# Performance work log

Hardware: AMD Instinct MI355X
Metric: run time of the kernel (lower is better)

Reference implementation:

```python
import jax, jax.numpy as jnp
import numpy as np

B, T, N, D_IN = 2, 64, 64, 512
HID, L, H = 256, 2, 4
C = HID // H  # 64 per-head channels
NEG_SLOPE = 0.2
LN_EPS = 1e-5


def setup_inputs() -> dict:
    key = jax.random.key(0)
    ks = jax.random.split(key, 8)
    s_in = 1.0 / np.sqrt(D_IN)
    s_h = 1.0 / np.sqrt(HID)
    s_c = 1.0 / np.sqrt(C)
    return {
        "x": jax.random.normal(ks[0], (B, T, N, D_IN), jnp.float32),
        "person_mask": jax.random.randint(ks[1], (B, T, N), 0, 2) > 0,
        "W_in": (jax.random.normal(ks[2], (D_IN, HID)) * s_in).astype(jnp.float32),
        "b_in": jnp.zeros((HID,), jnp.float32),
        "Wl": (jax.random.normal(ks[3], (L, HID, HID)) * s_h).astype(jnp.float32),
        "bl": jnp.zeros((L, HID), jnp.float32),
        "Wr": (jax.random.normal(ks[4], (L, HID, HID)) * s_h).astype(jnp.float32),
        "br": jnp.zeros((L, HID), jnp.float32),
        "att": (jax.random.normal(ks[5], (L, H, C)) * s_c).astype(jnp.float32),
        "out_bias": jnp.zeros((L, HID), jnp.float32),
        "ln_scale": jnp.ones((L, HID), jnp.float32),
        "ln_bias": jnp.zeros((L, HID), jnp.float32),
    }


def _layernorm(x, g, b):
    mu = jnp.mean(x, axis=-1, keepdims=True)
    var = jnp.mean(jnp.square(x - mu), axis=-1, keepdims=True)
    return (x - mu) * jax.lax.rsqrt(var + LN_EPS) * g + b


def _gatv2_layer(h, allowed, Wl, bl, Wr, br, att, ob):
    # h: [bt, N, HID]; allowed: [bt, N, N] bool (edge j->i at [b,i,j])
    bt, n, _ = h.shape
    xl = (h @ Wl + bl).reshape(bt, n, H, C)  # source features (messages)
    xr = (h @ Wr + br).reshape(bt, n, H, C)  # target features
    # GATv2 logit: e_ij = a . leaky_relu(xr_i + xl_j), per head
    s = xr[:, :, None, :, :] + xl[:, None, :, :, :]  # [bt, i, j, H, C]
    e = jnp.einsum('bijhc,hc->bijh', jax.nn.leaky_relu(s, NEG_SLOPE), att)
    e = jnp.where(allowed[..., None], e, -1e9)
    alpha = jax.nn.softmax(e, axis=2)  # segment softmax over incoming edges j
    out = jnp.einsum('bijh,bjhc->bihc', alpha, xl)  # weighted scatter-sum
    return out.reshape(bt, n, H * C) + ob


def _forward(x, person_mask, W_in, b_in, Wl, bl, Wr, br, att, out_bias, ln_scale, ln_bias):
    b, t, n, _ = x.shape
    bt = b * t
    h = (x @ W_in + b_in).reshape(bt, n, HID)
    m = person_mask.reshape(bt, n)
    # edges: all pairs among masked nodes (incl. diag) + self loops for every node
    allowed = (m[:, :, None] & m[:, None, :]) | jnp.eye(n, dtype=bool)[None]
    hi = h
    for li in range(L):
        res = hi
        g = _gatv2_layer(hi, allowed, Wl[li], bl[li], Wr[li], br[li], att[li], out_bias[li])
        g = jax.nn.elu(g)  # dropout is identity in eval mode
        g = _layernorm(g, ln_scale[li], ln_bias[li])
        hi = g + res  # use_residual=True
        hi = jnp.where(m[:, :, None], hi, 0.0)
    # graphs with <=1 masked node are skipped (pass through projected features)
    keep = (jnp.sum(m, axis=-1) > 1)[:, None, None]
    out = jnp.where(keep, hi, h)
    return out.reshape(b, t, n, HID)


def reference(x, person_mask, W_in, b_in, Wl, bl, Wr, br, att, out_bias, ln_scale, ln_bias):
    return _forward(x, person_mask, W_in, b_in, Wl, bl, Wr, br, att, out_bias, ln_scale, ln_bias)
```

## Files before the change

kernel.cpp:

```cpp
#include <hip/hip_runtime.h>
#include <hip/hip_bf16.h>

#define BT_G   128
#define NND    64
#define D_IN_  512
#define HID_   256
#define NH     4
#define NCH    64
#define NROWS  8192
#define LN_EPS_    1e-5f

typedef __hip_bfloat16 bf16;
typedef __attribute__((ext_vector_type(8))) short short8;
typedef __attribute__((ext_vector_type(4))) float float4v;

__device__ __forceinline__ float toF(bf16 x) { return __bfloat162float(x); }

__global__ __launch_bounds__(256) void transpose_all_kernel(
    const float* __restrict__ W_in, const float* __restrict__ Wl,
    const float* __restrict__ Wr, const unsigned int* __restrict__ mw,
    bf16* __restrict__ WTin, bf16* __restrict__ WlrT, int* __restrict__ mout) {
    const int z = blockIdx.z;
    const int tid = threadIdx.x;
    if (z == 5) {
        if (blockIdx.x || blockIdx.y) return;
        __shared__ int okInt, okF32, okB16, okByte;
        if (tid == 0) { okInt = 1; okF32 = 1; okB16 = 1; okByte = 1; }
        __syncthreads();
        int aI = 1, aF = 1, aB = 1, aC = 1;
        for (int i = tid; i < 2048; i += 256) {
            unsigned w = mw[i];
            aI &= (w <= 1u);
            aF &= (w == 0u || w == 0x3F800000u);
            unsigned lo = w & 0xFFFFu, hi = w >> 16;
            aB &= ((lo == 0u || lo == 0x3F80u) && (hi == 0u || hi == 0x3F80u));
            aC &= (((w | (w >> 8) | (w >> 16) | (w >> 24)) & 0xFEu) == 0u);
        }
        if (!aI) atomicAnd(&okInt, 0);
        if (!aF) atomicAnd(&okF32, 0);
        if (!aB) atomicAnd(&okB16, 0);
        if (!aC) atomicAnd(&okByte, 0);
        __syncthreads();
        const int layout = (okInt || okF32) ? 0 : (okB16 ? 2 : (okByte ? 3 : 0));
        for (int i = tid; i < NROWS; i += 256) {
            int v;
            if (layout == 2)      v = (((const unsigned short*)mw)[i] != 0);
            else if (layout == 3) v = (((const unsigned char*)mw)[i] != 0);
            else                  v = (mw[i] != 0u);
            mout[i] = v;
        }
        return;
    }
    __shared__ float t[32][33];
    const float* src; bf16* dst; int K;
    if (z == 0)      { src = W_in;                 dst = WTin;                    K = 512; }
    else if (z <= 2) { src = Wl + (z - 1) * 65536; dst = WlrT + (z - 1) * 131072; K = 256; }
    else             { src = Wr + (z - 3) * 65536; dst = WlrT + (z - 3) * 131072 + 256 * 256; K = 256; }
    const int n0 = blockIdx.x * 32, k0 = blockIdx.y * 32;
    if (k0 >= K) return;
    const int tx = tid & 31, ty = tid >> 5;
    #pragma unroll
    for (int i = 0; i < 4; ++i)
        t[ty + 8 * i][tx] = src[(size_t)(k0 + ty + 8 * i) * 256 + n0 + tx];
    __syncthreads();
    #pragma unroll
    for (int i = 0; i < 4; ++i)
        dst[(size_t)(n0 + ty + 8 * i) * K + k0 + tx] =
            __float2bfloat16(t[tx][ty + 8 * i]);
}

__global__ __launch_bounds__(256) void gemm_in_kernel(
    const float* __restrict__ A, const bf16* __restrict__ BT,
    const float* __restrict__ bias, float* __restrict__ Cf,
    bf16* __restrict__ Cb16)
{
    __shared__ bf16 As[64 * 72];
    __shared__ bf16 Bs[64 * 72];
    const int tid  = threadIdx.x;
    const int wave = tid >> 6, lane = tid & 63;
    const int quad = lane >> 4, l16 = lane & 15;
    const int m0 = blockIdx.y * 64, n0 = blockIdx.x * 64;
    const int wm = (wave & 1) * 32, wn = (wave >> 1) * 32;
    float4v acc[2][2] = {};
    const int r  = tid >> 2;
    const int cq = (tid & 3) * 16;

    for (int k0 = 0; k0 < D_IN_; k0 += 64) {
        const float* sa = A + (size_t)(m0 + r) * D_IN_ + k0 + cq;
        const float4 f0 = *(const float4*)(sa);
        const float4 f1 = *(const float4*)(sa + 4);
        const float4 f2 = *(const float4*)(sa + 8);
        const float4 f3 = *(const float4*)(sa + 12);
        const bf16* sb = BT + (size_t)(n0 + r) * D_IN_ + k0 + cq;
        const float4 b0 = *(const float4*)(sb);
        const float4 b1 = *(const float4*)(sb + 8);
        union { bf16 h[16]; float4 v[2]; } u;
        u.h[0]=__float2bfloat16(f0.x); u.h[1]=__float2bfloat16(f0.y);
        u.h[2]=__float2bfloat16(f0.z); u.h[3]=__float2bfloat16(f0.w);
        u.h[4]=__float2bfloat16(f1.x); u.h[5]=__float2bfloat16(f1.y);
        u.h[6]=__float2bfloat16(f1.z); u.h[7]=__float2bfloat16(f1.w);
        u.h[8]=__float2bfloat16(f2.x); u.h[9]=__float2bfloat16(f2.y);
        u.h[10]=__float2bfloat16(f2.z); u.h[11]=__float2bfloat16(f2.w);
        u.h[12]=__float2bfloat16(f3.x); u.h[13]=__float2bfloat16(f3.y);
        u.h[14]=__float2bfloat16(f3.z); u.h[15]=__float2bfloat16(f3.w);
        __syncthreads();
        *(float4*)(&As[r * 72 + cq])     = u.v[0];
        *(float4*)(&As[r * 72 + cq + 8]) = u.v[1];
        *(float4*)(&Bs[r * 72 + cq])     = b0;
        *(float4*)(&Bs[r * 72 + cq + 8]) = b1;
        __syncthreads();
        #pragma unroll
        for (int kk = 0; kk < 64; kk += 32) {
            short8 af[2], bf2[2];
            #pragma unroll
            for (int mi = 0; mi < 2; ++mi)
                af[mi] = *(const short8*)(&As[(wm + mi * 16 + l16) * 72 + kk + quad * 8]);
            #pragma unroll
            for (int ni = 0; ni < 2; ++ni)
                bf2[ni] = *(const short8*)(&Bs[(wn + ni * 16 + l16) * 72 + kk + quad * 8]);
            #pragma unroll
            for (int mi = 0; mi < 2; ++mi)
                #pragma unroll
                for (int ni = 0; ni < 2; ++ni)
                    acc[mi][ni] = __builtin_amdgcn_mfma_f32_16x16x32_bf16(
                        af[mi], bf2[ni], acc[mi][ni], 0, 0, 0);
        }
    }
    #pragma unroll
    for (int ni = 0; ni < 2; ++ni) {
        const int col = n0 + wn + ni * 16 + l16;
        const float bv = bias[col];
        #pragma unroll
        for (int mi = 0; mi < 2; ++mi)
            #pragma unroll
            for (int rr = 0; rr < 4; ++rr) {
                const int row = m0 + wm + mi * 16 + quad * 4 + rr;
                const float v = acc[mi][ni][rr] + bv;
                Cf[(size_t)row * HID_ + col] = v;
                Cb16[(size_t)row * HID_ + col] = __float2bfloat16(v);
            }
    }
}

__global__ __launch_bounds__(256) void gemm_mfma_kernel(
    const bf16* __restrict__ A, const bf16* __restrict__ BT,
    const float* __restrict__ bias0, const float* __restrict__ bias1,
    float* __restrict__ Ca, float* __restrict__ Cbf, int M, int K)
{
    __shared__ bf16 As[128 * 72];
    __shared__ bf16 Bs[64 * 72];
    const int tid  = threadIdx.x;
    const int wave = tid >> 6, lane = tid & 63;
    const int quad = lane >> 4, l16 = lane & 15;
    const int m0 = blockIdx.y * 128, n0g = blockIdx.x * 64;
    const int wm = (wave & 1) * 64, wn = (wave >> 1) * 32;
    float4v acc[4][2] = {};
    const int r  = tid >> 2;
    const int cq = (tid & 3) * 16;

    for (int k0 = 0; k0 < K; k0 += 64) {
        const bf16* sa0 = A  + (size_t)(m0 + r) * K + k0 + cq;
        const bf16* sa1 = sa0 + (size_t)64 * K;
        const bf16* sb  = BT + (size_t)(n0g + r) * K + k0 + cq;
        const float4 a00 = *(const float4*)(sa0);
        const float4 a01 = *(const float4*)(sa0 + 8);
        const float4 a10 = *(const float4*)(sa1);
        const float4 a11 = *(const float4*)(sa1 + 8);
        const float4 b0  = *(const float4*)(sb);
        const float4 b1  = *(const float4*)(sb + 8);
        __syncthreads();
        *(float4*)(&As[r * 72 + cq])            = a00;
        *(float4*)(&As[r * 72 + cq + 8])        = a01;
        *(float4*)(&As[(r + 64) * 72 + cq])     = a10;
        *(float4*)(&As[(r + 64) * 72 + cq + 8]) = a11;
        *(float4*)(&Bs[r * 72 + cq])            = b0;
        *(float4*)(&Bs[r * 72 + cq + 8])        = b1;
        __syncthreads();
        #pragma unroll
        for (int kk = 0; kk < 64; kk += 32) {
            short8 af[4], bf2[2];
            #pragma unroll
            for (int mi = 0; mi < 4; ++mi)
                af[mi] = *(const short8*)(&As[(wm + mi * 16 + l16) * 72 + kk + quad * 8]);
            #pragma unroll
            for (int ni = 0; ni < 2; ++ni)
                bf2[ni] = *(const short8*)(&Bs[(wn + ni * 16 + l16) * 72 + kk + quad * 8]);
            #pragma unroll
            for (int mi = 0; mi < 4; ++mi)
                #pragma unroll
                for (int ni = 0; ni < 2; ++ni)
                    acc[mi][ni] = __builtin_amdgcn_mfma_f32_16x16x32_bf16(
                        af[mi], bf2[ni], acc[mi][ni], 0, 0, 0);
        }
    }
    const bool loHalf = (n0g < 256);
    float* Co = loHalf ? Ca : Cbf;
    const float* bp = loHalf ? bias0 : bias1;
    const int cbase = loHalf ? n0g : (n0g - 256);
    #pragma unroll
    for (int ni = 0; ni < 2; ++ni) {
        const int col = cbase + wn + ni * 16 + l16;
        const float bv = bp[col];
        #pragma unroll
        for (int mi = 0; mi < 4; ++mi)
            #pragma unroll
            for (int rr = 0; rr < 4; ++rr) {
                const int row = m0 + wm + mi * 16 + quad * 4 + rr;
                Co[(size_t)row * 256 + col] = acc[mi][ni][rr] + bv;
            }
    }
}

__global__ __launch_bounds__(256) void attn_kernel(
    const float* xl, const float* xr, const float* att,
    const int* msk, float* g)
{
    __shared__ float xls [64][68];
    __shared__ float xlsT[64][68];
    __shared__ float xrsT[64][68];
    __shared__ float esT [64][68];
    __shared__ float av[64], P[64], Q[64], mxf[64], inv[64];
    __shared__ float pmax[4][64], psum[4][64];
    __shared__ int   ms[64];
    const int tid  = threadIdx.x;
    const int head = blockIdx.x, gr = blockIdx.y;
    const int ti = tid >> 4, tj = tid & 15;
    const int i0 = ti * 4, j0 = tj * 4;
    const float* xlg = xl + (size_t)gr * NND * HID_ + head * NCH;
    const float* xrg = xr + (size_t)gr * NND * HID_ + head * NCH;

    {
        const int r  = tid >> 2;
        const int c0 = (tid & 3) * 16;
        float a[4][4], b[4][4];
        #pragma unroll
        for (int k = 0; k < 4; ++k) {
            *(float4*)a[k] = *(const float4*)(xlg + r * HID_ + c0 + 4 * k);
            *(float4*)b[k] = *(const float4*)(xrg + r * HID_ + c0 + 4 * k);
        }
        #pragma unroll
        for (int k = 0; k < 4; ++k)
            *(float4*)&xls[r][c0 + 4 * k] = *(float4*)a[k];
        #pragma unroll
        for (int k = 0; k < 4; ++k)
            #pragma unroll
            for (int w = 0; w < 4; ++w) {
                xlsT[c0 + 4 * k + w][r] = a[k][w];
                xrsT[c0 + 4 * k + w][r] = b[k][w];
            }
    }
    if (tid < 64) {
        av[tid] = att[head * NCH + tid];
        ms[tid] = msk[gr * NND + tid];
    }
    __syncthreads();

    float aa[4][4] = {};
    for (int c = 0; c < 64; ++c) {
        float xr4[4], xl4[4];
        *(float4*)xr4 = *(const float4*)&xrsT[c][i0];
        *(float4*)xl4 = *(const float4*)&xlsT[c][j0];
        const float a = av[c];
        #pragma unroll
        for (int y = 0; y < 4; ++y)
            #pragma unroll
            for (int x = 0; x < 4; ++x)
                aa[y][x] = fmaf(a, fabsf(xr4[y] + xl4[x]), aa[y][x]);
    }
    if (tid < 64) {
        float s = 0.f;
        for (int c = 0; c < 64; ++c) s = fmaf(av[c], xrsT[c][tid], s);
        P[tid] = s;
    } else if (tid < 128) {
        const int j = tid - 64;
        float s = 0.f;
        for (int c = 0; c < 64; ++c) s = fmaf(av[c], xlsT[c][j], s);
        Q[j] = s;
    }
    __syncthreads();

    {
        float Pv[4], Qv[4]; int mi4[4], mj4[4];
        #pragma unroll
        for (int y = 0; y < 4; ++y) { Pv[y] = P[i0 + y]; mi4[y] = ms[i0 + y]; }
        #pragma unroll
        for (int x = 0; x < 4; ++x) { Qv[x] = Q[j0 + x]; mj4[x] = ms[j0 + x]; }
        #pragma unroll
        for (int x = 0; x < 4; ++x) {
            float col[4];
            #pragma unroll
            for (int y = 0; y < 4; ++y) {
                float e = fmaf(0.4f, aa[y][x], 0.6f * (Pv[y] + Qv[x]));
                const bool allowed = (mi4[y] && mj4[x]) || (i0 + y == j0 + x);
                col[y] = allowed ? e : -1e9f;
            }
            *(float4*)&esT[j0 + x][i0] = *(float4*)col;
        }
    }
    __syncthreads();

    {
        const int si = tid & 63, q = tid >> 6;
        float mx = -1e30f;
        #pragma unroll
        for (int k = 0; k < 16; ++k) mx = fmaxf(mx, esT[16 * q + k][si]);
        pmax[q][si] = mx;
    }
    __syncthreads();
    if (tid < 64)
        mxf[tid] = fmaxf(fmaxf(pmax[0][tid], pmax[1][tid]),
                         fmaxf(pmax[2][tid], pmax[3][tid]));
    __syncthreads();
    {
        const int si = tid & 63, q = tid >> 6;
        const float mx = mxf[si];
        float s = 0.f;
        #pragma unroll
        for (int k = 0; k < 16; ++k) {
            const float ev = __expf(esT[16 * q + k][si] - mx);
            esT[16 * q + k][si] = ev;
            s += ev;
        }
        psum[q][si] = s;
    }
    __syncthreads();
    if (tid < 64)
        inv[tid] = 1.f / (psum[0][tid] + psum[1][tid] + psum[2][tid] + psum[3][tid]);
    __syncthreads();

    {
        const int c0 = j0;
        float oa[4][4] = {};
        for (int j = 0; j < 64; ++j) {
            float al[4], xv[4];
            *(float4*)al = *(const float4*)&esT[j][i0];
            *(float4*)xv = *(const float4*)&xls[j][c0];
            #pragma unroll
            for (int y = 0; y < 4; ++y)
                #pragma unroll
                for (int x = 0; x < 4; ++x)
                    oa[y][x] = fmaf(al[y], xv[x], oa[y][x]);
        }
        #pragma unroll
        for (int y = 0; y < 4; ++y) {
            const float iv = inv[i0 + y];
            float o[4];
            #pragma unroll
            for (int x = 0; x < 4; ++x) o[x] = oa[y][x] * iv;
            float* go = g + (size_t)(gr * NND + i0 + y) * HID_ + head * NCH + c0;
            *(float4*)go = *(float4*)o;
        }
    }
}

__global__ __launch_bounds__(256) void epilogue_kernel(
    const float* __restrict__ g, const float* res,
    const float* __restrict__ ob, const float* __restrict__ lns,
    const float* __restrict__ lnb, const int* __restrict__ msk,
    float* hout, bf16* hb, int finalSel)
{
    const int lane = threadIdx.x & 63;
    const int wave = threadIdx.x >> 6;
    const int m = blockIdx.x * 4 + wave;
    if (finalSel) {
        const int gr = m >> 6;
        const int mv = msk[gr * NND + lane];
        const unsigned long long bal = __ballot(mv != 0);
        if (__popcll(bal) <= 1) return;
    }
    const float* grow = g + (size_t)m * HID_;
    float v[4];
    float sum = 0.f;
    #pragma unroll
    for (int q = 0; q < 4; ++q) {
        const int c = q * 64 + lane;
        float x = grow[c] + ob[c];
        x = x > 0.f ? x : (__expf(x) - 1.f);
        v[q] = x; sum += x;
    }
    #pragma unroll
    for (int off = 1; off < 64; off <<= 1) sum += __shfl_xor(sum, off);
    const float mu = sum * (1.f / 256.f);
    float vs = 0.f;
    #pragma unroll
    for (int q = 0; q < 4; ++q) { const float d = v[q] - mu; vs += d * d; }
    #pragma unroll
    for (int off = 1; off < 64; off <<= 1) vs += __shfl_xor(vs, off);
    const float rstd = rsqrtf(vs * (1.f / 256.f) + LN_EPS_);
    const int mnode = msk[m];
    const float* rrow = res + (size_t)m * HID_;
    float* ho = hout + (size_t)m * HID_;
    #pragma unroll
    for (int q = 0; q < 4; ++q) {
        const int c = q * 64 + lane;
        float y = (v[q] - mu) * rstd * lns[c] + lnb[c];
        y += rrow[c];
        y = mnode ? y : 0.f;
        ho[c] = y;
        if (hb) hb[(size_t)m * HID_ + c] = __float2bfloat16(y);
    }
}

extern "C" void kernel_launch(void* const* d_in, const int* in_sizes, int n_in,
                              void* d_out, int out_size, void* d_ws, size_t ws_size,
                              hipStream_t stream) {
    const float* x    = (const float*)d_in[0];
    const float* W_in = (const float*)d_in[2];
    const float* b_in = (const float*)d_in[3];
    const float* Wl   = (const float*)d_in[4];
    const float* bl   = (const float*)d_in[5];
    const float* Wr   = (const float*)d_in[6];
    const float* br   = (const float*)d_in[7];
    const float* att  = (const float*)d_in[8];
    const float* ob   = (const float*)d_in[9];
    const float* lns  = (const float*)d_in[10];
    const float* lnb  = (const float*)d_in[11];
    float* out = (float*)d_out;

    char* w = (char*)d_ws;
    int*   mcan = (int*)w;                      w += 32768;
    float* h    = (float*)w;                    w += (size_t)NROWS * HID_ * 4;
    float* xlb  = (float*)w;                    w += (size_t)NROWS * HID_ * 4;
    float* xrb  = (float*)w;                    w += (size_t)NROWS * HID_ * 4;
    bf16*  hxb  = (bf16*)w;                     w += (size_t)NROWS * HID_ * 2;
    bf16*  WTin = (bf16*)w;                     w += (size_t)D_IN_ * HID_ * 2;
    bf16*  WlrT = (bf16*)w;
    float* gb   = xrb;

    transpose_all_kernel<<<dim3(8, 16, 6), 256, 0, stream>>>(
        W_in, Wl, Wr, (const unsigned int*)d_in[1], WTin, WlrT, mcan);

    gemm_in_kernel<<<dim3(HID_ / 64, NROWS / 64), 256, 0, stream>>>(
        x, WTin, b_in, out, hxb);

    for (int li = 0; li < 2; ++li) {
        const float* resf = (li == 0) ? out : h;
        gemm_mfma_kernel<<<dim3(512 / 64, NROWS / 128), 256, 0, stream>>>(
            hxb, WlrT + (size_t)li * 512 * HID_, bl + li * HID_, br + li * HID_,
            xlb, xrb, NROWS, HID_);
        attn_kernel<<<dim3(NH, BT_G), 256, 0, stream>>>(
            xlb, xrb, att + li * NH * NCH, mcan, gb);
        if (li == 0) {
            epilogue_kernel<<<NROWS / 4, 256, 0, stream>>>(
                gb, resf, ob, lns, lnb, mcan, h, hxb, 0);
        } else {
            epilogue_kernel<<<NROWS / 4, 256, 0, stream>>>(
                gb, resf, ob + HID_, lns + HID_, lnb + HID_, mcan,
                out, (bf16*)nullptr, 1);
        }
    }

    (void)in_sizes; (void)n_in; (void)out_size; (void)ws_size;
}
```

Measured before the change: 176.8 us.

## Fuse all stages into one persistent cooperative kernel with grid syncs

Replaces the eight separate launches (transpose, input GEMM, and per-layer GEMM, attention and epilogue) with a single cooperative kernel of 256 blocks. Each stage runs as a grid-stride loop over work units, separated by grid.sync, with a union of per-stage shared-memory layouts. The goal is to remove per-launch overhead and tail gaps between kernels. In exchange it adds grid-wide barrier cost, caps the grid at one persistent wave of blocks, and sizes shared memory for the largest stage. The mask loading is also simplified to assume a 32-bit element layout, and a multi-kernel fallback path is kept in case the cooperative launch fails.

Result: slower. 458.9 us (+159.5%).

```diff
diff --git a/kernel.cpp b/kernel.cpp
--- a/kernel.cpp
+++ b/kernel.cpp
@@ -1,123 +1,112 @@
 #include <hip/hip_runtime.h>
 #include <hip/hip_bf16.h>
-
-#define BT_G   128
+#include <hip/hip_cooperative_groups.h>
+
+namespace cg = cooperative_groups;
+
 #define NND    64
 #define D_IN_  512
 #define HID_   256
 #define NH     4
 #define NCH    64
 #define NROWS  8192
-#define LN_EPS_    1e-5f
+#define LN_EPS_ 1e-5f
+#define CGRID  256
 
 typedef __hip_bfloat16 bf16;
 typedef __attribute__((ext_vector_type(8))) short short8;
 typedef __attribute__((ext_vector_type(4))) float float4v;
 
-__device__ __forceinline__ float toF(bf16 x) { return __bfloat162float(x); }
-
-__global__ __launch_bounds__(256) void transpose_all_kernel(
-    const float* __restrict__ W_in, const float* __restrict__ Wl,
-    const float* __restrict__ Wr, const unsigned int* __restrict__ mw,
-    bf16* __restrict__ WTin, bf16* __restrict__ WlrT, int* __restrict__ mout) {
-    const int z = blockIdx.z;
+struct TrS { float t[32][33]; };
+struct G1S { bf16 As[64 * 72]; bf16 Bs[64 * 72]; };
+struct G2S { bf16 As[128 * 72]; bf16 Bs[64 * 72]; };
+struct AtS {
+    float xls [64][68];
+    float xlsT[64][68];
+    float xrsT[64][68];
+    float esT [64][68];
+    float av[64], P[64], Q[64], mxf[64], inv[64];
+    float pmax[4][64], psum[4][64];
+    int   ms[64];
+};
+union SharedU { TrS tr; G1S g1; G2S g2; AtS at; };
+
+
+__device__ __forceinline__ void phase_transpose(
+    int u, TrS& sh, const float* W_in, const float* Wl, const float* Wr,
+    const unsigned int* mw, bf16* WTin, bf16* WlrT, int* mcan)
+{
     const int tid = threadIdx.x;
-    if (z == 5) {
-        if (blockIdx.x || blockIdx.y) return;
-        __shared__ int okInt, okF32, okB16, okByte;
-        if (tid == 0) { okInt = 1; okF32 = 1; okB16 = 1; okByte = 1; }
-        __syncthreads();
-        int aI = 1, aF = 1, aB = 1, aC = 1;
-        for (int i = tid; i < 2048; i += 256) {
-            unsigned w = mw[i];
-            aI &= (w <= 1u);
-            aF &= (w == 0u || w == 0x3F800000u);
-            unsigned lo = w & 0xFFFFu, hi = w >> 16;
-            aB &= ((lo == 0u || lo == 0x3F80u) && (hi == 0u || hi == 0x3F80u));
-            aC &= (((w | (w >> 8) | (w >> 16) | (w >> 24)) & 0xFEu) == 0u);
-        }
-        if (!aI) atomicAnd(&okInt, 0);
-        if (!aF) atomicAnd(&okF32, 0);
-        if (!aB) atomicAnd(&okB16, 0);
-        if (!aC) atomicAnd(&okByte, 0);
-        __syncthreads();
-        const int layout = (okInt || okF32) ? 0 : (okB16 ? 2 : (okByte ? 3 : 0));
-        for (int i = tid; i < NROWS; i += 256) {
-            int v;
-            if (layout == 2)      v = (((const unsigned short*)mw)[i] != 0);
-            else if (layout == 3) v = (((const unsigned char*)mw)[i] != 0);
-            else                  v = (mw[i] != 0u);
-            mout[i] = v;
-        }
+    if (u == 384) {
+        for (int i = tid; i < NROWS; i += 256) mcan[i] = (mw[i] != 0u);
         return;
     }
-    __shared__ float t[32][33];
-    const float* src; bf16* dst; int K;
-    if (z == 0)      { src = W_in;                 dst = WTin;                    K = 512; }
-    else if (z <= 2) { src = Wl + (z - 1) * 65536; dst = WlrT + (z - 1) * 131072; K = 256; }
-    else             { src = Wr + (z - 3) * 65536; dst = WlrT + (z - 3) * 131072 + 256 * 256; K = 256; }
-    const int n0 = blockIdx.x * 32, k0 = blockIdx.y * 32;
-    if (k0 >= K) return;
+    const float* src; bf16* dst; int K, t;
+    if (u < 128) { src = W_in; dst = WTin; K = 512; t = u; }
+    else {
+        const int idx = u - 128, mat = idx >> 6;
+        t = idx & 63; K = 256;
+        const int li = mat & 1; const bool isR = (mat >= 2);
+        src = (isR ? Wr : Wl) + li * 65536;
+        dst = WlrT + li * 131072 + (isR ? 65536 : 0);
+    }
+    const int n0 = (t & 7) * 32, k0 = (t >> 3) * 32;
     const int tx = tid & 31, ty = tid >> 5;
     #pragma unroll
     for (int i = 0; i < 4; ++i)
-        t[ty + 8 * i][tx] = src[(size_t)(k0 + ty + 8 * i) * 256 + n0 + tx];
+        sh.t[ty + 8 * i][tx] = src[(size_t)(k0 + ty + 8 * i) * 256 + n0 + tx];
     __syncthreads();
     #pragma unroll
     for (int i = 0; i < 4; ++i)
         dst[(size_t)(n0 + ty + 8 * i) * K + k0 + tx] =
-            __float2bfloat16(t[tx][ty + 8 * i]);
-}
-
-__global__ __launch_bounds__(256) void gemm_in_kernel(
-    const float* __restrict__ A, const bf16* __restrict__ BT,
-    const float* __restrict__ bias, float* __restrict__ Cf,
-    bf16* __restrict__ Cb16)
+            __float2bfloat16(sh.t[tx][ty + 8 * i]);
+}
+
+__device__ __forceinline__ void phase_gemm_in(
+    int u, G1S& sh, const float* x, const bf16* WTin, const float* b_in,
+    float* out, bf16* hxb)
 {
-    __shared__ bf16 As[64 * 72];
-    __shared__ bf16 Bs[64 * 72];
-    const int tid  = threadIdx.x;
+    const int tid = threadIdx.x;
     const int wave = tid >> 6, lane = tid & 63;
     const int quad = lane >> 4, l16 = lane & 15;
-    const int m0 = blockIdx.y * 64, n0 = blockIdx.x * 64;
+    const int m0 = (u >> 2) * 64, n0 = (u & 3) * 64;
     const int wm = (wave & 1) * 32, wn = (wave >> 1) * 32;
     float4v acc[2][2] = {};
     const int r  = tid >> 2;
     const int cq = (tid & 3) * 16;
-
     for (int k0 = 0; k0 < D_IN_; k0 += 64) {
-        const float* sa = A + (size_t)(m0 + r) * D_IN_ + k0 + cq;
+        const float* sa = x + (size_t)(m0 + r) * D_IN_ + k0 + cq;
         const float4 f0 = *(const float4*)(sa);
         const float4 f1 = *(const float4*)(sa + 4);
         const float4 f2 = *(const float4*)(sa + 8);
         const float4 f3 = *(const float4*)(sa + 12);
-        const bf16* sb = BT + (size_t)(n0 + r) * D_IN_ + k0 + cq;
+        const bf16* sb = WTin + (size_t)(n0 + r) * D_IN_ + k0 + cq;
         const float4 b0 = *(const float4*)(sb);
         const float4 b1 = *(const float4*)(sb + 8);
-        union { bf16 h[16]; float4 v[2]; } u;
-        u.h[0]=__float2bfloat16(f0.x); u.h[1]=__float2bfloat16(f0.y);
-        u.h[2]=__float2bfloat16(f0.z); u.h[3]=__float2bfloat16(f0.w);
-        u.h[4]=__float2bfloat16(f1.x); u.h[5]=__float2bfloat16(f1.y);
-        u.h[6]=__float2bfloat16(f1.z); u.h[7]=__float2bfloat16(f1.w);
-        u.h[8]=__float2bfloat16(f2.x); u.h[9]=__float2bfloat16(f2.y);
-        u.h[10]=__float2bfloat16(f2.z); u.h[11]=__float2bfloat16(f2.w);
-        u.h[12]=__float2bfloat16(f3.x); u.h[13]=__float2bfloat16(f3.y);
-        u.h[14]=__float2bfloat16(f3.z); u.h[15]=__float2bfloat16(f3.w);
+        union { bf16 hh[16]; float4 v[2]; } uu;
+        uu.hh[0]=__float2bfloat16(f0.x); uu.hh[1]=__float2bfloat16(f0.y);
+        uu.hh[2]=__float2bfloat16(f0.z); uu.hh[3]=__float2bfloat16(f0.w);
+        uu.hh[4]=__float2bfloat16(f1.x); uu.hh[5]=__float2bfloat16(f1.y);
+        uu.hh[6]=__float2bfloat16(f1.z); uu.hh[7]=__float2bfloat16(f1.w);
+        uu.hh[8]=__float2bfloat16(f2.x); uu.hh[9]=__float2bfloat16(f2.y);
+        uu.hh[10]=__float2bfloat16(f2.z); uu.hh[11]=__float2bfloat16(f2.w);
+        uu.hh[12]=__float2bfloat16(f3.x); uu.hh[13]=__float2bfloat16(f3.y);
+        uu.hh[14]=__float2bfloat16(f3.z); uu.hh[15]=__float2bfloat16(f3.w);
         __syncthreads();
-        *(float4*)(&As[r * 72 + cq])     = u.v[0];
-        *(float4*)(&As[r * 72 + cq + 8]) = u.v[1];
-        *(float4*)(&Bs[r * 72 + cq])     = b0;
-        *(float4*)(&Bs[r * 72 + cq + 8]) = b1;
+        *(float4*)(&sh.As[r * 72 + cq])     = uu.v[0];
+        *(float4*)(&sh.As[r * 72 + cq + 8]) = uu.v[1];
+        *(float4*)(&sh.Bs[r * 72 + cq])     = b0;
+        *(float4*)(&sh.Bs[r * 72 + cq + 8]) = b1;
         __syncthreads();
         #pragma unroll
         for (int kk = 0; kk < 64; kk += 32) {
             short8 af[2], bf2[2];
             #pragma unroll
             for (int mi = 0; mi < 2; ++mi)
-                af[mi] = *(const short8*)(&As[(wm + mi * 16 + l16) * 72 + kk + quad * 8]);
+                af[mi] = *(const short8*)(&sh.As[(wm + mi * 16 + l16) * 72 + kk + quad * 8]);
             #pragma unroll
             for (int ni = 0; ni < 2; ++ni)
-                bf2[ni] = *(const short8*)(&Bs[(wn + ni * 16 + l16) * 72 + kk + quad * 8]);
+                bf2[ni] = *(const short8*)(&sh.Bs[(wn + ni * 16 + l16) * 72 + kk + quad * 8]);
             #pragma unroll
             for (int mi = 0; mi < 2; ++mi)
                 #pragma unroll
@@ -129,39 +118,35 @@
     #pragma unroll
     for (int ni = 0; ni < 2; ++ni) {
         const int col = n0 + wn + ni * 16 + l16;
-        const float bv = bias[col];
+        const float bv = b_in[col];
         #pragma unroll
         for (int mi = 0; mi < 2; ++mi)
             #pragma unroll
             for (int rr = 0; rr < 4; ++rr) {
                 const int row = m0 + wm + mi * 16 + quad * 4 + rr;
                 const float v = acc[mi][ni][rr] + bv;
-                Cf[(size_t)row * HID_ + col] = v;
-                Cb16[(size_t)row * HID_ + col] = __float2bfloat16(v);
+                out[(size_t)row * HID_ + col] = v;
+                hxb[(size_t)row * HID_ + col] = __float2bfloat16(v);
             }
     }
 }
 
-__global__ __launch_bounds__(256) void gemm_mfma_kernel(
-    const bf16* __restrict__ A, const bf16* __restrict__ BT,
-    const float* __restrict__ bias0, const float* __restrict__ bias1,
-    float* __restrict__ Ca, float* __restrict__ Cbf, int M, int K)
+__device__ __forceinline__ void phase_gemm_lr(
+    int u, G2S& sh, const bf16* hxb, const bf16* BT,
+    const float* bias0, const float* bias1, float* xlb, float* xrb)
 {
-    __shared__ bf16 As[128 * 72];
-    __shared__ bf16 Bs[64 * 72];
-    const int tid  = threadIdx.x;
+    const int tid = threadIdx.x;
     const int wave = tid >> 6, lane = tid & 63;
     const int quad = lane >> 4, l16 = lane & 15;
-    const int m0 = blockIdx.y * 128, n0g = blockIdx.x * 64;
+    const int m0 = (u >> 3) * 128, n0g = (u & 7) * 64;
     const int wm = (wave & 1) * 64, wn = (wave >> 1) * 32;
     float4v acc[4][2] = {};
     const int r  = tid >> 2;
     const int cq = (tid & 3) * 16;
-
-    for (int k0 = 0; k0 < K; k0 += 64) {
-        const bf16* sa0 = A  + (size_t)(m0 + r) * K + k0 + cq;
-        const bf16* sa1 = sa0 + (size_t)64 * K;
-        const bf16* sb  = BT + (size_t)(n0g + r) * K + k0 + cq;
+    for (int k0 = 0; k0 < HID_; k0 += 64) {
+        const bf16* sa0 = hxb + (size_t)(m0 + r) * HID_ + k0 + cq;
+        const bf16* sa1 = sa0 + (size_t)64 * HID_;
+        const bf16* sb  = BT + (size_t)(n0g + r) * HID_ + k0 + cq;
         const float4 a00 = *(const float4*)(sa0);
         const float4 a01 = *(const float4*)(sa0 + 8);
         const float4 a10 = *(const float4*)(sa1);
@@ -169,22 +154,22 @@
         const float4 b0  = *(const float4*)(sb);
         const float4 b1  = *(const float4*)(sb + 8);
         __syncthreads();
-        *(float4*)(&As[r * 72 + cq])            = a00;
-        *(float4*)(&As[r * 72 + cq + 8])        = a01;
-        *(float4*)(&As[(r + 64) * 72 + cq])     = a10;
-        *(float4*)(&As[(r + 64) * 72 + cq + 8]) = a11;
-        *(float4*)(&Bs[r * 72 + cq])            = b0;
-        *(float4*)(&Bs[r * 72 + cq + 8])        = b1;
+        *(float4*)(&sh.As[r * 72 + cq])            = a00;
+        *(float4*)(&sh.As[r * 72 + cq + 8])        = a01;
+        *(float4*)(&sh.As[(r + 64) * 72 + cq])     = a10;
+        *(float4*)(&sh.As[(r + 64) * 72 + cq + 8]) = a11;
+        *(float4*)(&sh.Bs[r * 72 + cq])            = b0;
+        *(float4*)(&sh.Bs[r * 72 + cq + 8])        = b1;
         __syncthreads();
         #pragma unroll
         for (int kk = 0; kk < 64; kk += 32) {
             short8 af[4], bf2[2];
             #pragma unroll
             for (int mi = 0; mi < 4; ++mi)
-                af[mi] = *(const short8*)(&As[(wm + mi * 16 + l16) * 72 + kk + quad * 8]);
+                af[mi] = *(const short8*)(&sh.As[(wm + mi * 16 + l16) * 72 + kk + quad * 8]);
             #pragma unroll
             for (int ni = 0; ni < 2; ++ni)
-                bf2[ni] = *(const short8*)(&Bs[(wn + ni * 16 + l16) * 72 + kk + quad * 8]);
+                bf2[ni] = *(const short8*)(&sh.Bs[(wn + ni * 16 + l16) * 72 + kk + quad * 8]);
             #pragma unroll
             for (int mi = 0; mi < 4; ++mi)
                 #pragma unroll
@@ -194,7 +179,7 @@
         }
     }
     const bool loHalf = (n0g < 256);
-    float* Co = loHalf ? Ca : Cbf;
+    float* Co = loHalf ? xlb : xrb;
     const float* bp = loHalf ? bias0 : bias1;
     const int cbase = loHalf ? n0g : (n0g - 256);
     #pragma unroll
@@ -211,24 +196,16 @@
     }
 }
 
-__global__ __launch_bounds__(256) void attn_kernel(
-    const float* xl, const float* xr, const float* att,
-    const int* msk, float* g)
+__device__ __forceinline__ void phase_attn(
+    int u, AtS& sh, const float* xlb, const float* xrb, const float* attL,
+    const int* mcan, float* gb)
 {
-    __shared__ float xls [64][68];
-    __shared__ float xlsT[64][68];
-    __shared__ float xrsT[64][68];
-    __shared__ float esT [64][68];
-    __shared__ float av[64], P[64], Q[64], mxf[64], inv[64];
-    __shared__ float pmax[4][64], psum[4][64];
-    __shared__ int   ms[64];
-    const int tid  = threadIdx.x;
-    const int head = blockIdx.x, gr = blockIdx.y;
+    const int tid = threadIdx.x;
+    const int head = u & 3, gr = u >> 2;
     const int ti = tid >> 4, tj = tid & 15;
     const int i0 = ti * 4, j0 = tj * 4;
-    const float* xlg = xl + (size_t)gr * NND * HID_ + head * NCH;
-    const float* xrg = xr + (size_t)gr * NND * HID_ + head * NCH;
-
+    const float* xlg = xlb + (size_t)gr * NND * HID_ + head * NCH;
+    const float* xrg = xrb + (size_t)gr * NND * HID_ + head * NCH;
     {
         const int r  = tid >> 2;
         const int c0 = (tid & 3) * 16;
@@ -240,61 +217,61 @@
         }
         #pragma unroll
         for (int k = 0; k < 4; ++k)
-            *(float4*)&xls[r][c0 + 4 * k] = *(float4*)a[k];
+            *(float4*)&sh.xls[r][c0 + 4 * k] = *(float4*)a[k];
         #pragma unroll
         for (int k = 0; k < 4; ++k)
             #pragma unroll
             for (int w = 0; w < 4; ++w) {
-                xlsT[c0 + 4 * k + w][r] = a[k][w];
-                xrsT[c0 + 4 * k + w][r] = b[k][w];
+                sh.xlsT[c0 + 4 * k + w][r] = a[k][w];
+                sh.xrsT[c0 + 4 * k + w][r] = b[k][w];
             }
     }
     if (tid < 64) {
-        av[tid] = att[head * NCH + tid];
-        ms[tid] = msk[gr * NND + tid];
+        sh.av[tid] = attL[head * NCH + tid];
+        sh.ms[tid] = mcan[gr * NND + tid];
     }
     __syncthreads();
 
     float aa[4][4] = {};
     for (int c = 0; c < 64; ++c) {
         float xr4[4], xl4[4];
-        *(float4*)xr4 = *(const float4*)&xrsT[c][i0];
-        *(float4*)xl4 = *(const float4*)&xlsT[c][j0];
-        const float a = av[c];
+        *(float4*)xr4 = *(const float4*)&sh.xrsT[c][i0];
+        *(float4*)xl4 = *(const float4*)&sh.xlsT[c][j0];
+        const float a = sh.av[c];
         #pragma unroll
         for (int y = 0; y < 4; ++y)
             #pragma unroll
-            for (int x = 0; x < 4; ++x)
-                aa[y][x] = fmaf(a, fabsf(xr4[y] + xl4[x]), aa[y][x]);
+            for (int xx = 0; xx < 4; ++xx)
+                aa[y][xx] = fmaf(a, fabsf(xr4[y] + xl4[xx]), aa[y][xx]);
     }
     if (tid < 64) {
         float s = 0.f;
-        for (int c = 0; c < 64; ++c) s = fmaf(av[c], xrsT[c][tid], s);
-        P[tid] = s;
+        for (int c = 0; c < 64; ++c) s = fmaf(sh.av[c], sh.xrsT[c][tid], s);
+        sh.P[tid] = s;
     } else if (tid < 128) {
         const int j = tid - 64;
         float s = 0.f;
-        for (int c = 0; c < 64; ++c) s = fmaf(av[c], xlsT[c][j], s);
-        Q[j] = s;
+        for (int c = 0; c < 64; ++c) s = fmaf(sh.av[c], sh.xlsT[c][j], s);
+        sh.Q[j] = s;
     }
     __syncthreads();
 
     {
         float Pv[4], Qv[4]; int mi4[4], mj4[4];
         #pragma unroll
-        for (int y = 0; y < 4; ++y) { Pv[y] = P[i0 + y]; mi4[y] = ms[i0 + y]; }
-        #pragma unroll
-        for (int x = 0; x < 4; ++x) { Qv[x] = Q[j0 + x]; mj4[x] = ms[j0 + x]; }
-        #pragma unroll
-        for (int x = 0; x < 4; ++x) {
+        for (int y = 0; y < 4; ++y) { Pv[y] = sh.P[i0 + y]; mi4[y] = sh.ms[i0 + y]; }
+        #pragma unroll
+        for (int xx = 0; xx < 4; ++xx) { Qv[xx] = sh.Q[j0 + xx]; mj4[xx] = sh.ms[j0 + xx]; }
+        #pragma unroll
+        for (int xx = 0; xx < 4; ++xx) {
             float col[4];
             #pragma unroll
             for (int y = 0; y < 4; ++y) {
-                float e = fmaf(0.4f, aa[y][x], 0.6f * (Pv[y] + Qv[x]));
-                const bool allowed = (mi4[y] && mj4[x]) || (i0 + y == j0 + x);
+                float e = fmaf(0.4f, aa[y][xx], 0.6f * (Pv[y] + Qv[xx]));
+                const bool allowed = (mi4[y] && mj4[xx]) || (i0 + y == j0 + xx);
                 col[y] = allowed ? e : -1e9f;
             }
-            *(float4*)&esT[j0 + x][i0] = *(float4*)col;
+            *(float4*)&sh.esT[j0 + xx][i0] = *(float4*)col;
         }
     }
     __syncthreads();
@@ -303,29 +280,30 @@
         const int si = tid & 63, q = tid >> 6;
         float mx = -1e30f;
         #pragma unroll
-        for (int k = 0; k < 16; ++k) mx = fmaxf(mx, esT[16 * q + k][si]);
-        pmax[q][si] = mx;
+        for (int k = 0; k < 16; ++k) mx = fmaxf(mx, sh.esT[16 * q + k][si]);
+        sh.pmax[q][si] = mx;
     }
     __syncthreads();
     if (tid < 64)
-        mxf[tid] = fmaxf(fmaxf(pmax[0][tid], pmax[1][tid]),
-                         fmaxf(pmax[2][tid], pmax[3][tid]));
+        sh.mxf[tid] = fmaxf(fmaxf(sh.pmax[0][tid], sh.pmax[1][tid]),
+                            fmaxf(sh.pmax[2][tid], sh.pmax[3][tid]));
     __syncthreads();
     {
         const int si = tid & 63, q = tid >> 6;
-        const float mx = mxf[si];
+        const float mx = sh.mxf[si];
         float s = 0.f;
         #pragma unroll
         for (int k = 0; k < 16; ++k) {
-            const float ev = __expf(esT[16 * q + k][si] - mx);
-            esT[16 * q + k][si] = ev;
+            const float ev = __expf(sh.esT[16 * q + k][si] - mx);
+            sh.esT[16 * q + k][si] = ev;
             s += ev;
         }
-        psum[q][si] = s;
+        sh.psum[q][si] = s;
     }
     __syncthreads();
     if (tid < 64)
-        inv[tid] = 1.f / (psum[0][tid] + psum[1][tid] + psum[2][tid] + psum[3][tid]);
+        sh.inv[tid] = 1.f / (sh.psum[0][tid] + sh.psum[1][tid] +
+                             sh.psum[2][tid] + sh.psum[3][tid]);
     __syncthreads();
 
     {
@@ -333,50 +311,48 @@
         float oa[4][4] = {};
         for (int j = 0; j < 64; ++j) {
             float al[4], xv[4];
-            *(float4*)al = *(const float4*)&esT[j][i0];
-            *(float4*)xv = *(const float4*)&xls[j][c0];
+            *(float4*)al = *(const float4*)&sh.esT[j][i0];
+            *(float4*)xv = *(const float4*)&sh.xls[j][c0];
             #pragma unroll
             for (int y = 0; y < 4; ++y)
                 #pragma unroll
-                for (int x = 0; x < 4; ++x)
-                    oa[y][x] = fmaf(al[y], xv[x], oa[y][x]);
+                for (int xx = 0; xx < 4; ++xx)
+                    oa[y][xx] = fmaf(al[y], xv[xx], oa[y][xx]);
         }
         #pragma unroll
         for (int y = 0; y < 4; ++y) {
-            const float iv = inv[i0 + y];
+            const float iv = sh.inv[i0 + y];
             float o[4];
             #pragma unroll
-            for (int x = 0; x < 4; ++x) o[x] = oa[y][x] * iv;
-            float* go = g + (size_t)(gr * NND + i0 + y) * HID_ + head * NCH + c0;
+            for (int xx = 0; xx < 4; ++xx) o[xx] = oa[y][xx] * iv;
+            float* go = gb + (size_t)(gr * NND + i0 + y) * HID_ + head * NCH + c0;
             *(float4*)go = *(float4*)o;
         }
     }
 }
 
-__global__ __launch_bounds__(256) void epilogue_kernel(
-    const float* __restrict__ g, const float* res,
-    const float* __restrict__ ob, const float* __restrict__ lns,
-    const float* __restrict__ lnb, const int* __restrict__ msk,
+__device__ __forceinline__ void phase_epi(
+    int u, const float* gb, const float* res, const float* obp,
+    const float* lsp, const float* lbp, const int* mcan,
     float* hout, bf16* hb, int finalSel)
 {
     const int lane = threadIdx.x & 63;
     const int wave = threadIdx.x >> 6;
-    const int m = blockIdx.x * 4 + wave;
+    const int m = u * 4 + wave;
     if (finalSel) {
         const int gr = m >> 6;
-        const int mv = msk[gr * NND + lane];
-        const unsigned long long bal = __ballot(mv != 0);
+        const unsigned long long bal = __ballot(mcan[gr * NND + lane] != 0);
         if (__popcll(bal) <= 1) return;
     }
-    const float* grow = g + (size_t)m * HID_;
+    const float* grow = gb + (size_t)m * HID_;
     float v[4];
     float sum = 0.f;
     #pragma unroll
     for (int q = 0; q < 4; ++q) {
         const int c = q * 64 + lane;
-        float x = grow[c] + ob[c];
-        x = x > 0.f ? x : (__expf(x) - 1.f);
-        v[q] = x; sum += x;
+        float xv = grow[c] + obp[c];
+        xv = xv > 0.f ? xv : (__expf(xv) - 1.f);
+        v[q] = xv; sum += xv;
     }
     #pragma unroll
     for (int off = 1; off < 64; off <<= 1) sum += __shfl_xor(sum, off);
@@ -387,13 +363,13 @@
     #pragma unroll
     for (int off = 1; off < 64; off <<= 1) vs += __shfl_xor(vs, off);
     const float rstd = rsqrtf(vs * (1.f / 256.f) + LN_EPS_);
-    const int mnode = msk[m];
+    const int mnode = mcan[m];
     const float* rrow = res + (size_t)m * HID_;
     float* ho = hout + (size_t)m * HID_;
     #pragma unroll
     for (int q = 0; q < 4; ++q) {
         const int c = q * 64 + lane;
-        float y = (v[q] - mu) * rstd * lns[c] + lnb[c];
+        float y = (v[q] - mu) * rstd * lsp[c] + lbp[c];
         y += rrow[c];
         y = mnode ? y : 0.f;
         ho[c] = y;
@@ -401,10 +377,90 @@
     }
 }
 
+__global__ __launch_bounds__(256, 2) void fused_kernel(
+    const float* x, const unsigned int* mw,
+    const float* W_in, const float* b_in,
+    const float* Wl, const float* bl,
+    const float* Wr, const float* br,
+    const float* att, const float* ob,
+    const float* lns, const float* lnb,
+    float* out, int* mcan, float* h, float* xlb, float* xrb,
+    bf16* hxb, bf16* WTin, bf16* WlrT)
+{
+    __shared__ SharedU sh;
+    cg::grid_group grid = cg::this_grid();
+    const int bid = blockIdx.x;
+
+    for (int u = bid; u < 385; u += CGRID) {
+        phase_transpose(u, sh.tr, W_in, Wl, Wr, mw, WTin, WlrT, mcan);
+        __syncthreads();
+    }
+    grid.sync();
+
+    for (int u = bid; u < 512; u += CGRID) {
+        phase_gemm_in(u, sh.g1, x, WTin, b_in, out, hxb);
+        __syncthreads();
+    }
+    grid.sync();
+
+    for (int li = 0; li < 2; ++li) {
+        const bf16* BT = WlrT + (size_t)li * 131072;
+        for (int u = bid; u < 512; u += CGRID) {
+            phase_gemm_lr(u, sh.g2, hxb, BT, bl + li * HID_, br + li * HID_,
+                          xlb, xrb);
+            __syncthreads();
+        }
+        grid.sync();
+        for (int u = bid; u < 512; u += CGRID) {
+            phase_attn(u, sh.at, xlb, xrb, att + li * NH * NCH, mcan, xrb);
+            __syncthreads();
+        }
+        grid.sync();
+        const float* res = (li == 0) ? out : h;
+        float* hout = (li == 0) ? h : out;
+        for (int u = bid; u < 2048; u += CGRID)
+            phase_epi(u, xrb, res, ob + li * HID_, lns + li * HID_,
+                      lnb + li * HID_, mcan, hout,
+                      (li == 0) ? hxb : (bf16*)nullptr, li);
+        if (li == 0) grid.sync();
+    }
+}
+
+__global__ __launch_bounds__(256) void k_transpose(
+    const float* W_in, const float* Wl, const float* Wr,
+    const unsigned int* mw, bf16* WTin, bf16* WlrT, int* mcan) {
+    __shared__ TrS sh;
+    phase_transpose(blockIdx.x, sh, W_in, Wl, Wr, mw, WTin, WlrT, mcan);
+}
+__global__ __launch_bounds__(256) void k_gemm_in(
+    const float* x, const bf16* WTin, const float* b_in,
+    float* out, bf16* hxb) {
+    __shared__ G1S sh;
+    phase_gemm_in(blockIdx.x, sh, x, WTin, b_in, out, hxb);
+}
+__global__ __launch_bounds__(256) void k_gemm_lr(
+    const bf16* hxb, const bf16* BT, const float* bias0, const float* bias1,
+    float* xlb, float* xrb) {
+    __shared__ G2S sh;
+    phase_gemm_lr(blockIdx.x, sh, hxb, BT, bias0, bias1, xlb, xrb);
+}
+__global__ __launch_bounds__(256) void k_attn(
+    const float* xlb, const float* xrb, const float* attL,
+    const int* mcan, float* gb) {
+    __shared__ AtS sh;
+    phase_attn(blockIdx.x, sh, xlb, xrb, attL, mcan, gb);
+}
+__global__ __launch_bounds__(256) void k_epi(
+    const float* gb, const float* res, const float* obp, const float* lsp,
+    const float* lbp, const int* mcan, float* hout, bf16* hb, int finalSel) {
+    phase_epi(blockIdx.x, gb, res, obp, lsp, lbp, mcan, hout, hb, finalSel);
+}
+
 extern "C" void kernel_launch(void* const* d_in, const int* in_sizes, int n_in,
                               void* d_out, int out_size, void* d_ws, size_t ws_size,
                               hipStream_t stream) {
     const float* x    = (const float*)d_in[0];
+    const unsigned int* mw = (const unsigned int*)d_in[1];
     const float* W_in = (const float*)d_in[2];
     const float* b_in = (const float*)d_in[3];
     const float* Wl   = (const float*)d_in[4];
@@ -425,28 +481,27 @@
     bf16*  hxb  = (bf16*)w;                     w += (size_t)NROWS * HID_ * 2;
     bf16*  WTin = (bf16*)w;                     w += (size_t)D_IN_ * HID_ * 2;
     bf16*  WlrT = (bf16*)w;
-    float* gb   = xrb;
-
-    transpose_all_kernel<<<dim3(8, 16, 6), 256, 0, stream>>>(
-        W_in, Wl, Wr, (const unsigned int*)d_in[1], WTin, WlrT, mcan);
-
-    gemm_in_kernel<<<dim3(HID_ / 64, NROWS / 64), 256, 0, stream>>>(
-        x, WTin, b_in, out, hxb);
-
-    for (int li = 0; li < 2; ++li) {
-        const float* resf = (li == 0) ? out : h;
-        gemm_mfma_kernel<<<dim3(512 / 64, NROWS / 128), 256, 0, stream>>>(
-            hxb, WlrT + (size_t)li * 512 * HID_, bl + li * HID_, br + li * HID_,
-            xlb, xrb, NROWS, HID_);
-        attn_kernel<<<dim3(NH, BT_G), 256, 0, stream>>>(
-            xlb, xrb, att + li * NH * NCH, mcan, gb);
-        if (li == 0) {
-            epilogue_kernel<<<NROWS / 4, 256, 0, stream>>>(
-                gb, resf, ob, lns, lnb, mcan, h, hxb, 0);
-        } else {
-            epilogue_kernel<<<NROWS / 4, 256, 0, stream>>>(
-                gb, resf, ob + HID_, lns + HID_, lnb + HID_, mcan,
-                out, (bf16*)nullptr, 1);
+
+    void* args[] = { &x, &mw, &W_in, &b_in, &Wl, &bl, &Wr, &br, &att, &ob,
+                     &lns, &lnb, &out, &mcan, &h, &xlb, &xrb, &hxb, &WTin, &WlrT };
+    hipError_t err = hipLaunchCooperativeKernel(
+        (const void*)fused_kernel, dim3(CGRID), dim3(256), args, 0, stream);
+
+    if (err != hipSuccess) {
+        (void)hipGetLastError();
+        k_transpose<<<385, 256, 0, stream>>>(W_in, Wl, Wr, mw, WTin, WlrT, mcan);
+        k_gemm_in<<<512, 256, 0, stream>>>(x, WTin, b_in, out, hxb);
+        for (int li = 0; li < 2; ++li) {
+            k_gemm_lr<<<512, 256, 0, stream>>>(
+                hxb, WlrT + (size_t)li * 131072, bl + li * HID_, br + li * HID_,
+                xlb, xrb);
+            k_attn<<<512, 256, 0, stream>>>(
+                xlb, xrb, att + li * NH * NCH, mcan, xrb);
+            const float* res = (li == 0) ? out : h;
+            float* hout = (li == 0) ? h : out;
+            k_epi<<<2048, 256, 0, stream>>>(
+                xrb, res, ob + li * HID_, lns + li * HID_, lnb + li * HID_,
+                mcan, hout, (li == 0) ? hxb : (bf16*)nullptr, li);
         }
     }
 
```
